# Optimization experiments

Hardware: AMD Instinct MI355X
Metric: run time of the kernel (lower is better)

## Reference

```python
import jax, jax.numpy as jnp
import numpy as np

B, E, H, A = 16384, 128, 256, 20


def _xavier(key, shape):
    scale = (2.0 / (shape[0] + shape[1])) ** 0.5
    return (jax.random.normal(key, shape, jnp.float32) * scale).astype(jnp.float32)


def setup_inputs() -> dict:
    key = jax.random.key(0)
    ks = jax.random.split(key, 16)
    d = {
        'x1': jax.random.normal(ks[0], (B, E), jnp.float32),
        'x2': jax.random.normal(ks[1], (B, A, E), jnp.float32),
        'h': jax.random.normal(ks[2], (B, H), jnp.float32),
        'c1': jax.random.normal(ks[3], (B, H), jnp.float32),
        'c2': jax.random.normal(ks[4], (B, H), jnp.float32),
    }
    gate_names = ['f', 'i', 'c', 'o']
    for j, n in enumerate(gate_names):
        d[f'W1_{n}'] = _xavier(ks[5 + 2 * j], (H + E, H))
        d[f'W2_{n}'] = _xavier(ks[6 + 2 * j], (H + E, H))
        d[f'b1_{n}'] = jnp.zeros((H,), jnp.float32)
        d[f'b2_{n}'] = jnp.zeros((H,), jnp.float32)
    d['W_attn'] = _xavier(ks[13], (H + 2 * E, 1))
    return d


def reference(x1, x2, h, c1, c2,
              W1_f, W2_f, b1_f, b2_f,
              W1_i, W2_i, b1_i, b2_i,
              W1_c, W2_c, b1_c, b2_c,
              W1_o, W2_o, b1_o, b2_o,
              W_attn):
    hx1 = jnp.concatenate([h, x1], axis=1)                    # [B, H+E]
    # attention: score_a = [h, x1, x2_a] @ W_attn ; split W_attn to vectorize
    base = hx1 @ W_attn[:H + E, 0]                            # [B]
    scores = base[:, None] + jnp.einsum('bae,e->ba', x2, W_attn[H + E:, 0])  # [B, A]
    attn = jax.nn.softmax(scores, axis=1)
    x2m = jnp.einsum('ba,bae->be', attn, x2)                  # [B, E]
    hx2 = jnp.concatenate([h, x2m], axis=1)                   # [B, H+E]

    f1 = jax.nn.sigmoid(hx1 @ W1_f + b1_f)
    f2 = jax.nn.sigmoid(hx2 @ W2_f + b2_f)
    i1 = jax.nn.sigmoid(hx1 @ W1_i + b1_i)
    i2 = jax.nn.sigmoid(hx2 @ W2_i + b2_i)
    c1t = jnp.tanh(hx1 @ W1_c + b1_c)
    c2t = jnp.tanh(hx2 @ W2_c + b2_c)
    c1n = f1 * c1 + i1 * c1t
    c2n = f2 * c2 + i2 * c2t

    o1 = hx1 @ W1_o + b1_o
    o2 = hx2 @ W2_o + b2_o
    # exp(o1)/(exp(o1)+exp(o2)) mixing == softmax over the 2-cell axis (stable form)
    g = jax.nn.softmax(jnp.stack([o1, o2], axis=0), axis=0)
    h_new = g[0] * jnp.tanh(c1n) + g[1] * jnp.tanh(c2n)
    return (h_new, c1n, c2n)
```

## Files before the change

kernel.cpp:

```cpp
#include <hip/hip_runtime.h>
#include <hip/hip_bf16.h>

#define B_SZ 16384
#define E_SZ 128
#define H_SZ 256
#define A_SZ 20
#define K_SZ 384
#define BH   (B_SZ * H_SZ)

typedef __attribute__((ext_vector_type(8))) short  short8v;
typedef __attribute__((ext_vector_type(4))) float  f32x4;
typedef __attribute__((ext_vector_type(2))) float  f32x2;
typedef __attribute__((ext_vector_type(4))) unsigned short ushort4v;
typedef __attribute__((ext_vector_type(2))) unsigned short ushort2v;

__device__ __forceinline__ unsigned short f2bf(float f) {
    union { float f; unsigned u; } v; v.f = f;
    unsigned r = v.u + 0x7fffu + ((v.u >> 16) & 1u);
    return (unsigned short)(r >> 16);
}

__device__ __forceinline__ float wsum(float v) {
    #pragma unroll
    for (int off = 32; off > 0; off >>= 1) v += __shfl_xor(v, off, 64);
    return v;
}

__device__ __forceinline__ float tanh_fast(float x) {
    float cx = fminf(fmaxf(x, -15.f), 15.f);
    float t  = __expf(2.f * cx);
    return (t - 1.f) * __builtin_amdgcn_rcpf(t + 1.f);
}
__device__ __forceinline__ float sigm_fast(float x) {
    float cx = fminf(fmaxf(x, -30.f), 30.f);
    return __builtin_amdgcn_rcpf(1.f + __expf(-cx));
}

struct Ptr8 { const float* p[8]; };

__global__ __launch_bounds__(256) void attn_pack(
    const float* __restrict__ x1, const float* __restrict__ x2,
    const float* __restrict__ h,  const float* __restrict__ wa,
    unsigned short* __restrict__ Hb, unsigned short* __restrict__ A1x,
    unsigned short* __restrict__ A2x)
{
    const int row  = blockIdx.x * 4 + (threadIdx.x >> 6);
    const int lane = threadIdx.x & 63;

    const f32x4 hv   = *(const f32x4*)(h  + (size_t)row * H_SZ + 4 * lane);
    const f32x2 x1v  = *(const f32x2*)(x1 + (size_t)row * E_SZ + 2 * lane);
    const f32x4 wah  = *(const f32x4*)(wa + 4 * lane);
    const f32x2 wax1 = *(const f32x2*)(wa + H_SZ + 2 * lane);
    const f32x2 wax2 = *(const f32x2*)(wa + H_SZ + E_SZ + 2 * lane);

    float base = hv.x * wah.x + hv.y * wah.y + hv.z * wah.z + hv.w * wah.w
               + x1v.x * wax1.x + x1v.y * wax1.y;

    f32x2 xv[A_SZ];
    float sp[A_SZ];
    const float* x2r = x2 + (size_t)row * A_SZ * E_SZ;
    #pragma unroll
    for (int a = 0; a < A_SZ; ++a) {
        xv[a] = *(const f32x2*)(x2r + a * E_SZ + 2 * lane);
        sp[a] = xv[a].x * wax2.x + xv[a].y * wax2.y;
    }

    base = wsum(base);
    #pragma unroll
    for (int a = 0; a < A_SZ; ++a) sp[a] = wsum(sp[a]) + base;

    float mx = sp[0];
    #pragma unroll
    for (int a = 1; a < A_SZ; ++a) mx = fmaxf(mx, sp[a]);
    float s = 0.0f;
    #pragma unroll
    for (int a = 0; a < A_SZ; ++a) { sp[a] = __expf(sp[a] - mx); s += sp[a]; }
    const float inv = 1.0f / s;

    float m0 = 0.0f, m1 = 0.0f;
    #pragma unroll
    for (int a = 0; a < A_SZ; ++a) { m0 += sp[a] * xv[a].x; m1 += sp[a] * xv[a].y; }
    m0 *= inv; m1 *= inv;

    ushort4v hb;
    hb.x = f2bf(hv.x); hb.y = f2bf(hv.y); hb.z = f2bf(hv.z); hb.w = f2bf(hv.w);
    *(ushort4v*)(Hb + (size_t)row * H_SZ + 4 * lane) = hb;
    ushort2v x1b; x1b.x = f2bf(x1v.x); x1b.y = f2bf(x1v.y);
    *(ushort2v*)(A1x + (size_t)row * E_SZ + 2 * lane) = x1b;
    ushort2v mb; mb.x = f2bf(m0); mb.y = f2bf(m1);
    *(ushort2v*)(A2x + (size_t)row * E_SZ + 2 * lane) = mb;
}

__global__ __launch_bounds__(256) void pack_w(Ptr8 ws, unsigned short* __restrict__ Wt)
{
    const int g = blockIdx.z, nt = blockIdx.y, kt = blockIdx.x;
    __shared__ float tile[64][65];
    const float* W = ws.p[g];
    const int c = threadIdx.x & 63, r0 = threadIdx.x >> 6;
    #pragma unroll
    for (int i = 0; i < 16; ++i) {
        int r = r0 + 4 * i;
        tile[r][c] = W[(size_t)(kt * 64 + r) * H_SZ + nt * 64 + c];
    }
    __syncthreads();
    #pragma unroll
    for (int i = 0; i < 16; ++i) {
        int rr = r0 + 4 * i;
        const int hcol = nt * 64 + rr;
        const int nn = ((hcol >> 5) << 8) + g * 32 + (hcol & 31);
        Wt[(size_t)nn * K_SZ + kt * 64 + c] = f2bf(tile[c][rr]);
    }
}

__global__ __launch_bounds__(512, 1) void gemm_ep(
    const unsigned short* __restrict__ Hb, const unsigned short* __restrict__ A1x,
    const unsigned short* __restrict__ A2x, const unsigned short* __restrict__ Wt,
    Ptr8 bias, const float* __restrict__ c1, const float* __restrict__ c2,
    float* __restrict__ out)
{
    __shared__ char smem[131072];
    const int tid = threadIdx.x, w = tid >> 6, lane = tid & 63;
    const int d = blockIdx.x;
    const int rb  = (d & 7) * 16 + (d >> 6);
    const int hcb = (d >> 3) & 7;
    const int row0 = rb * 128, hcol0 = hcb * 32;
    const int fr = lane & 15, hi = lane >> 4;
    const int wM = w >> 2, wN = w & 3;

    const unsigned short* Bpan = Wt + (size_t)hcb * 256 * K_SZ;
    const int lr = lane >> 3, sl = lane & 7;

    const int hcin = tid & 31, rgrp = tid >> 5;
    float c1p[8], c2p[8], bia[8];
    #pragma unroll
    for (int rr = 0; rr < 8; ++rr) {
        const int R = rgrp * 8 + rr;
        c1p[rr] = c1[(size_t)(row0 + R) * H_SZ + hcol0 + hcin];
        c2p[rr] = c2[(size_t)(row0 + R) * H_SZ + hcol0 + hcin];
    }
    #pragma unroll
    for (int g = 0; g < 8; ++g) bia[g] = bias.p[g][hcol0 + hcin];

    auto glds = [&](const unsigned short* src, int dstoff) {
        __builtin_amdgcn_global_load_lds(
            (const __attribute__((address_space(1))) unsigned int*)src,
            (__attribute__((address_space(3))) unsigned int*)(smem + dstoff), 16, 0, 0);
    };
    auto stage = [&](int ks, int b) {
        const int bufb = b * 65536;
        #pragma unroll
        for (int j = 0; j < 4; ++j) {
            const int C = j * 64 + w * 8 + lr;
            glds(Bpan + (size_t)C * K_SZ + ks * 64 + ((sl ^ (C & 7)) << 3),
                 bufb + 32768 + j * 8192 + w * 1024);
        }
        if (ks < 4) {
            #pragma unroll
            for (int i = 0; i < 2; ++i) {
                const int R = i * 64 + w * 8 + lr;
                glds(Hb + (size_t)(row0 + R) * H_SZ + ks * 64 + ((sl ^ (R & 7)) << 3),
                     bufb + i * 8192 + w * 1024);
            }
        } else {
            const int ko = (ks - 4) * 64;
            #pragma unroll
            for (int i = 0; i < 2; ++i) {
                const int R = i * 64 + w * 8 + lr;
                const int sw = (sl ^ (R & 7)) << 3;
                glds(A1x + (size_t)(row0 + R) * E_SZ + ko + sw,
                     bufb + i * 8192 + w * 1024);
                glds(A2x + (size_t)(row0 + R) * E_SZ + ko + sw,
                     bufb + 16384 + i * 8192 + w * 1024);
            }
        }
    };

    f32x4 acc[4][4];
    #pragma unroll
    for (int mi = 0; mi < 4; ++mi)
        #pragma unroll
        for (int ni = 0; ni < 4; ++ni) acc[mi][ni] = (f32x4){0.f, 0.f, 0.f, 0.f};

    stage(0, 0);
    for (int ks = 0; ks < 6; ++ks) {
        __syncthreads();
        if (ks < 5) stage(ks + 1, (ks + 1) & 1);
        const char* bb = smem + (ks & 1) * 65536;
        const int apo = (ks >= 4 && wN >= 2) ? 16384 : 0;
        #pragma unroll
        for (int kk = 0; kk < 2; ++kk) {
            short8v af[4], bf[4];
            #pragma unroll
            for (int mi = 0; mi < 4; ++mi) {
                const int R = wM * 64 + mi * 16 + fr;
                af[mi] = *(const short8v*)(bb + apo + R * 128 +
                                           ((((kk << 2) + hi) ^ (R & 7)) << 4));
            }
            #pragma unroll
            for (int ni = 0; ni < 4; ++ni) {
                const int C = wN * 64 + ni * 16 + fr;
                bf[ni] = *(const short8v*)(bb + 32768 + C * 128 +
                                           ((((kk << 2) + hi) ^ (C & 7)) << 4));
            }
            #pragma unroll
            for (int mi = 0; mi < 4; ++mi)
                #pragma unroll
                for (int ni = 0; ni < 4; ++ni)
                    acc[mi][ni] = __builtin_amdgcn_mfma_f32_16x16x32_bf16(
                        af[mi], bf[ni], acc[mi][ni], 0, 0, 0);
        }
    }

    __syncthreads();
    float* gf = (float*)smem;
    #pragma unroll
    for (int mi = 0; mi < 4; ++mi)
        #pragma unroll
        for (int ni = 0; ni < 4; ++ni)
            #pragma unroll
            for (int j = 0; j < 4; ++j) {
                const int R   = wM * 64 + mi * 16 + hi * 4 + j;
                const int g   = wN * 2 + (ni >> 1);
                const int hc  = (ni & 1) * 16 + fr;
                const int hcr = (hc + (((R >> 2) & 3) << 3)) & 31;
                gf[(g * 128 + R) * 32 + hcr] = acc[mi][ni][j];
            }
    __syncthreads();

    #pragma unroll
    for (int rr = 0; rr < 8; ++rr) {
        const int R   = rgrp * 8 + rr;
        const int hcr = (hcin + (((R >> 2) & 3) << 3)) & 31;
        float G[8];
        #pragma unroll
        for (int g = 0; g < 8; ++g) G[g] = gf[(g * 128 + R) * 32 + hcr] + bia[g];

        const float f1  = sigm_fast(G[0]);
        const float i1  = sigm_fast(G[1]);
        const float c1t = tanh_fast(G[2]);
        const float f2  = sigm_fast(G[4]);
        const float i2  = sigm_fast(G[5]);
        const float c2t = tanh_fast(G[6]);
        const float c1n = f1 * c1p[rr] + i1 * c1t;
        const float c2n = f2 * c2p[rr] + i2 * c2t;
        const float g0  = sigm_fast(G[3] - G[7]);
        const float th1 = tanh_fast(c1n);
        const float th2 = tanh_fast(c2n);
        const float hn  = th2 + g0 * (th1 - th2);

        const size_t o0 = (size_t)(row0 + R) * H_SZ + hcol0 + hcin;
        out[o0]          = hn;
        out[BH + o0]     = c1n;
        out[2 * BH + o0] = c2n;
    }
}

extern "C" void kernel_launch(void* const* d_in, const int* in_sizes, int n_in,
                              void* d_out, int out_size, void* d_ws, size_t ws_size,
                              hipStream_t stream)
{
    const float* x1 = (const float*)d_in[0];
    const float* x2 = (const float*)d_in[1];
    const float* h  = (const float*)d_in[2];
    const float* c1 = (const float*)d_in[3];
    const float* c2 = (const float*)d_in[4];
    const float* wa = (const float*)d_in[21];

    Ptr8 wptr, bptr;
    wptr.p[0] = (const float*)d_in[5];  wptr.p[1] = (const float*)d_in[9];
    wptr.p[2] = (const float*)d_in[13]; wptr.p[3] = (const float*)d_in[17];
    wptr.p[4] = (const float*)d_in[6];  wptr.p[5] = (const float*)d_in[10];
    wptr.p[6] = (const float*)d_in[14]; wptr.p[7] = (const float*)d_in[18];
    bptr.p[0] = (const float*)d_in[7];  bptr.p[1] = (const float*)d_in[11];
    bptr.p[2] = (const float*)d_in[15]; bptr.p[3] = (const float*)d_in[19];
    bptr.p[4] = (const float*)d_in[8];  bptr.p[5] = (const float*)d_in[12];
    bptr.p[6] = (const float*)d_in[16]; bptr.p[7] = (const float*)d_in[20];

    char* ws = (char*)d_ws;
    unsigned short* Hb  = (unsigned short*)(ws);
    unsigned short* A1x = (unsigned short*)(ws + 8388608);
    unsigned short* A2x = (unsigned short*)(ws + 12582912);
    unsigned short* Wt  = (unsigned short*)(ws + 16777216);

    pack_w<<<dim3(6, 4, 8), 256, 0, stream>>>(wptr, Wt);
    attn_pack<<<B_SZ / 4, 256, 0, stream>>>(x1, x2, h, wa, Hb, A1x, A2x);
    gemm_ep<<<1024, 512, 0, stream>>>(Hb, A1x, A2x, Wt, bptr, c1, c2, (float*)d_out);
}
```

Before: 97.28 us.

## Restructure GEMM k-loop with split A/B staging, k-major LDS layout and priority hints

```diff
diff --git a/kernel.cpp b/kernel.cpp
--- a/kernel.cpp
+++ b/kernel.cpp
@@ -111,6 +111,8 @@
         Wt[(size_t)nn * K_SZ + kt * 64 + c] = f2bf(tile[c][rr]);
     }
 }
+
+#define WAITV(N) asm volatile("s_waitcnt vmcnt(" #N ")" ::: "memory")
 
 __global__ __launch_bounds__(512, 1) void gemm_ep(
     const unsigned short* __restrict__ Hb, const unsigned short* __restrict__ A1x,
@@ -128,9 +130,8 @@
     const int wM = w >> 2, wN = w & 3;
 
     const unsigned short* Bpan = Wt + (size_t)hcb * 256 * K_SZ;
-    const int lr = lane >> 3, sl = lane & 7;
-
     const int hcin = tid & 31, rgrp = tid >> 5;
+
     float c1p[8], c2p[8], bia[8];
     #pragma unroll
     for (int rr = 0; rr < 8; ++rr) {
@@ -146,31 +147,27 @@
             (const __attribute__((address_space(1))) unsigned int*)src,
             (__attribute__((address_space(3))) unsigned int*)(smem + dstoff), 16, 0, 0);
     };
-    auto stage = [&](int ks, int b) {
+    auto stageB = [&](int t, int b) {
         const int bufb = b * 65536;
         #pragma unroll
         for (int j = 0; j < 4; ++j) {
-            const int C = j * 64 + w * 8 + lr;
-            glds(Bpan + (size_t)C * K_SZ + ks * 64 + ((sl ^ (C & 7)) << 3),
-                 bufb + 32768 + j * 8192 + w * 1024);
+            const int o = j * 8192 + tid * 16;
+            const int kslot = o >> 12, C = (o >> 4) & 255;
+            glds(Bpan + (size_t)C * K_SZ + t * 64 + kslot * 8, bufb + 32768 + o);
         }
-        if (ks < 4) {
-            #pragma unroll
-            for (int i = 0; i < 2; ++i) {
-                const int R = i * 64 + w * 8 + lr;
-                glds(Hb + (size_t)(row0 + R) * H_SZ + ks * 64 + ((sl ^ (R & 7)) << 3),
-                     bufb + i * 8192 + w * 1024);
-            }
-        } else {
-            const int ko = (ks - 4) * 64;
-            #pragma unroll
-            for (int i = 0; i < 2; ++i) {
-                const int R = i * 64 + w * 8 + lr;
-                const int sw = (sl ^ (R & 7)) << 3;
-                glds(A1x + (size_t)(row0 + R) * E_SZ + ko + sw,
-                     bufb + i * 8192 + w * 1024);
-                glds(A2x + (size_t)(row0 + R) * E_SZ + ko + sw,
-                     bufb + 16384 + i * 8192 + w * 1024);
+    };
+    auto stageA = [&](int t, int b) {
+        const int bufb = b * 65536;
+        #pragma unroll
+        for (int i = 0; i < 2; ++i) {
+            const int o = i * 8192 + tid * 16;
+            const int kslot = o >> 11, R = (o >> 4) & 127;
+            if (t < 4) {
+                glds(Hb + (size_t)(row0 + R) * H_SZ + t * 64 + kslot * 8, bufb + o);
+            } else {
+                const int k = (t - 4) * 64 + kslot * 8;
+                glds(A1x + (size_t)(row0 + R) * E_SZ + k, bufb + o);
+                glds(A2x + (size_t)(row0 + R) * E_SZ + k, bufb + 16384 + o);
             }
         }
     };
@@ -181,34 +178,56 @@
         #pragma unroll
         for (int ni = 0; ni < 4; ++ni) acc[mi][ni] = (f32x4){0.f, 0.f, 0.f, 0.f};
 
-    stage(0, 0);
-    for (int ks = 0; ks < 6; ++ks) {
-        __syncthreads();
-        if (ks < 5) stage(ks + 1, (ks + 1) & 1);
-        const char* bb = smem + (ks & 1) * 65536;
-        const int apo = (ks >= 4 && wN >= 2) ? 16384 : 0;
-        #pragma unroll
-        for (int kk = 0; kk < 2; ++kk) {
+    stageB(0, 0);
+    stageA(0, 0);
+
+    #pragma unroll
+    for (int t = 0; t < 6; ++t) {
+        const char* bb = smem + (t & 1) * 65536;
+        const int apo = (t >= 4 && wN >= 2) ? 16384 : 0;
+        if (t < 5) { stageB(t + 1, (t + 1) & 1); WAITV(4); }
+        else       { WAITV(0); }
+        __builtin_amdgcn_s_barrier();
+        {
             short8v af[4], bf[4];
             #pragma unroll
-            for (int mi = 0; mi < 4; ++mi) {
-                const int R = wM * 64 + mi * 16 + fr;
-                af[mi] = *(const short8v*)(bb + apo + R * 128 +
-                                           ((((kk << 2) + hi) ^ (R & 7)) << 4));
-            }
-            #pragma unroll
-            for (int ni = 0; ni < 4; ++ni) {
-                const int C = wN * 64 + ni * 16 + fr;
-                bf[ni] = *(const short8v*)(bb + 32768 + C * 128 +
-                                           ((((kk << 2) + hi) ^ (C & 7)) << 4));
-            }
+            for (int mi = 0; mi < 4; ++mi)
+                af[mi] = *(const short8v*)(bb + apo + hi * 2048 +
+                                           (wM * 64 + mi * 16 + fr) * 16);
+            #pragma unroll
+            for (int ni = 0; ni < 4; ++ni)
+                bf[ni] = *(const short8v*)(bb + 32768 + hi * 4096 +
+                                           (wN * 64 + ni * 16 + fr) * 16);
+            __builtin_amdgcn_s_setprio(1);
             #pragma unroll
             for (int mi = 0; mi < 4; ++mi)
                 #pragma unroll
                 for (int ni = 0; ni < 4; ++ni)
                     acc[mi][ni] = __builtin_amdgcn_mfma_f32_16x16x32_bf16(
                         af[mi], bf[ni], acc[mi][ni], 0, 0, 0);
+            __builtin_amdgcn_s_setprio(0);
         }
+        if (t < 5) stageA(t + 1, (t + 1) & 1);
+        {
+            short8v af[4], bf[4];
+            #pragma unroll
+            for (int mi = 0; mi < 4; ++mi)
+                af[mi] = *(const short8v*)(bb + apo + (4 + hi) * 2048 +
+                                           (wM * 64 + mi * 16 + fr) * 16);
+            #pragma unroll
+            for (int ni = 0; ni < 4; ++ni)
+                bf[ni] = *(const short8v*)(bb + 32768 + (4 + hi) * 4096 +
+                                           (wN * 64 + ni * 16 + fr) * 16);
+            __builtin_amdgcn_s_setprio(1);
+            #pragma unroll
+            for (int mi = 0; mi < 4; ++mi)
+                #pragma unroll
+                for (int ni = 0; ni < 4; ++ni)
+                    acc[mi][ni] = __builtin_amdgcn_mfma_f32_16x16x32_bf16(
+                        af[mi], bf[ni], acc[mi][ni], 0, 0, 0);
+            __builtin_amdgcn_s_setprio(0);
+        }
+        __builtin_amdgcn_s_barrier();
     }
 
     __syncthreads();
```

Result: slower. 121.1 us (+24.5%).
